# Kernel optimization log

Hardware: AMD Instinct MI355X
Metric: run time of the kernel (lower is better)

The kernel has to match this reference:

```python
import jax, jax.numpy as jnp
import numpy as np

N, E, D_IN, D_H, D_OUT = 8000, 256000, 128, 128, 64
TEMP = 10.0       # config temperature.value (non-learnable)
WEIGHT = 1.0      # config weight.value (non-learnable)
LN_EPS = 1e-5


def _gcn_conv(x, W, b, src, dst, n):
    # PyG GCNConv: add self loops, sym-normalized aggregation, then bias.
    h = x @ W
    loop = jnp.arange(n)
    s = jnp.concatenate([src, loop])
    d = jnp.concatenate([dst, loop])
    deg = jnp.zeros((n,), h.dtype).at[d].add(1.0)
    dinv = jax.lax.rsqrt(jnp.maximum(deg, 1e-12))
    norm = dinv[s] * dinv[d]                       # [E+N]
    out = jax.ops.segment_sum(h[s] * norm[:, None], d, num_segments=n)
    return out + b


def _entropy_gradient(x, A, temperature, normalize):
    # E_i = 0.5 * sum_j A_ij ||x_i - x_j||^2  (dense adjacency, as in repo)
    sq = jnp.sum(x * x, axis=1)                    # [N]
    Ax = A @ x                                     # [N,d]
    deg = A.sum(axis=1)                            # [N]
    En = 0.5 * (deg * sq + A @ sq - 2.0 * jnp.sum(x * Ax, axis=1))
    if normalize:
        En = En / (jnp.max(En) + 1e-12)
    logits = -En / temperature
    P = jax.nn.softmax(logits)
    logP = jax.nn.log_softmax(logits)
    S = -jnp.sum(P * logP)
    c = P * (logP + S) / temperature               # dS/dE_k
    # dS/dx_i = c_i*(deg_i x_i - (Ax)_i) + (A^T c)_i x_i - (A^T (c*x))_i
    ATc = A.T @ c
    return (c[:, None] * (deg[:, None] * x - Ax)
            + ATc[:, None] * x - A.T @ (c[:, None] * x))


def _layer_norm(x, gamma, beta):
    mu = jnp.mean(x, axis=-1, keepdims=True)
    var = jnp.mean(jnp.square(x - mu), axis=-1, keepdims=True)
    return (x - mu) * jax.lax.rsqrt(var + LN_EPS) * gamma + beta


def setup_inputs() -> dict:
    key = jax.random.key(0)
    ks = jax.random.split(key, 6)
    def w(k, i, o):
        return jax.random.normal(k, (i, o), jnp.float32) / np.sqrt(i).astype(np.float32)
    return {
        "x": jax.random.normal(ks[0], (N, D_IN), jnp.float32),
        "edge_index": jax.random.randint(ks[1], (2, E), 0, N),
        "W1": w(ks[2], D_IN, D_H), "b1": jnp.zeros((D_H,), jnp.float32),
        "W2": w(ks[3], D_H, D_H), "b2": jnp.zeros((D_H,), jnp.float32),
        "W_out": w(ks[4], D_H, D_OUT), "b_out": jnp.zeros((D_OUT,), jnp.float32),
        "ln_gamma": jnp.ones((D_H,), jnp.float32),
        "ln_beta": jnp.zeros((D_H,), jnp.float32),
    }


def reference(x, edge_index, W1, b1, W2, b2, W_out, b_out, ln_gamma, ln_beta):
    n = x.shape[0]
    src, dst = edge_index[0], edge_index[1]
    # dense adjacency (to_dense_adj sums duplicate edges)
    A = jnp.zeros((n, n), x.dtype).at[src, dst].add(1.0)
    for W, b in ((W1, b1), (W2, b2)):
        h = _gcn_conv(x, W, b, src, dst, n)
        eg = jax.lax.stop_gradient(_entropy_gradient(h, A, TEMP, True))
        h = h + WEIGHT * eg
        h = jax.nn.relu(h)
        x = _layer_norm(h, ln_gamma, ln_beta)
    embedding = _gcn_conv(x, W_out, b_out, src, dst, n)
    return embedding
```

## Files before the change

kernel.cpp:

```cpp
#include <hip/hip_runtime.h>
#include <hip/hip_bf16.h>

#define DH 128

static constexpr float TEMP_ = 10.0f;
static constexpr float LN_EPS_ = 1e-5f;

__device__ __forceinline__ unsigned short f2bf(float f) {
  union { float f; unsigned int i; } v; v.f = f;
  unsigned int b = v.i + 0x7FFFu + ((v.i >> 16) & 1u);
  return (unsigned short)(b >> 16);
}
__device__ __forceinline__ void dec2(unsigned int u, float& lo, float& hi) {
  union { unsigned int i; float f; } a, b;
  a.i = u << 16; b.i = u & 0xFFFF0000u;
  lo = a.f; hi = b.f;
}
__device__ __forceinline__ void dec8(uint4 u, float* o) {
  dec2(u.x, o[0], o[1]); dec2(u.y, o[2], o[3]);
  dec2(u.z, o[4], o[5]); dec2(u.w, o[6], o[7]);
}
__device__ __forceinline__ unsigned int pack2(float lo, float hi) {
  return (unsigned int)f2bf(lo) | ((unsigned int)f2bf(hi) << 16);
}

__device__ __forceinline__ float grp_sum16(float v) {
  #pragma unroll
  for (int o = 8; o > 0; o >>= 1) v += __shfl_down(v, o, 16);
  return __shfl(v, 0, 16);
}

__device__ __forceinline__ float blkred(float v, bool mx, float* s4) {
  const int t = threadIdx.x;
  #pragma unroll
  for (int o = 32; o > 0; o >>= 1) {
    float u = __shfl_down(v, o, 64);
    v = mx ? fmaxf(v, u) : v + u;
  }
  __syncthreads();
  if ((t & 63) == 0) s4[t >> 6] = v;
  __syncthreads();
  float r = mx ? fmaxf(fmaxf(s4[0], s4[1]), fmaxf(s4[2], s4[3]))
               : (s4[0] + s4[1]) + (s4[2] + s4[3]);
  __syncthreads();
  return r;
}

__global__ __launch_bounds__(256) void k_gemm1_hist(const float* __restrict__ X,
                                                    const float* __restrict__ W,
                                                    unsigned short* __restrict__ Hb,
                                                    const int* __restrict__ ei, int E,
                                                    int* cnt_d, int* cnt_s, int NT) {
  __shared__ float Ws[64 * DH];
  __shared__ float xs[16 * 128];
  const int t = threadIdx.x;
  if ((int)blockIdx.x < NT) {
    const int row0 = blockIdx.x * 16;
    const float4* xg = (const float4*)(X + row0 * 128);
    float4* xs4 = (float4*)xs;
    xs4[t] = xg[t];
    xs4[t + 256] = xg[t + 256];
    const int c = t & 127, rg = t >> 7;
    float acc[8];
    #pragma unroll
    for (int r = 0; r < 8; ++r) acc[r] = 0.f;
    for (int kt = 0; kt < 2; ++kt) {
      __syncthreads();
      for (int i = t; i < 64 * DH; i += 256) Ws[i] = W[kt * 64 * DH + i];
      __syncthreads();
      for (int k = 0; k < 64; ++k) {
        float wv = Ws[k * DH + c];
        #pragma unroll
        for (int r = 0; r < 8; ++r)
          acc[r] += xs[(rg * 8 + r) * 128 + kt * 64 + k] * wv;
      }
    }
    #pragma unroll
    for (int r = 0; r < 8; ++r)
      Hb[(row0 + rg * 8 + r) * DH + c] = f2bf(acc[r]);
  } else {
    const int nb = gridDim.x - NT;
    for (int e = (blockIdx.x - NT) * 256 + t; e < E; e += nb * 256) {
      atomicAdd(&cnt_s[ei[e]], 1);
      atomicAdd(&cnt_d[ei[E + e]], 1);
    }
  }
}

__global__ __launch_bounds__(256) void k_scan_a(const int* __restrict__ cnt_d,
                                                const int* __restrict__ cnt_s,
                                                int* off_d, int* off_s, int* bsum,
                                                float* dinv, float* dego, int n) {
  __shared__ int ws4[4];
  const int t = threadIdx.x;
  const int dir = blockIdx.x >> 5, blk = blockIdx.x & 31;
  const int* cnt = dir ? cnt_s : cnt_d;
  int* off = dir ? off_s : off_d;
  const int NPB = (n + 31) >> 5;
  const int i = blk * NPB + t;
  const bool valid = (t < NPB) && (i < n);
  int tot = valid ? cnt[i] : 0;
  const int lane = t & 63, w = t >> 6;
  int v = tot;
  #pragma unroll
  for (int o = 1; o < 64; o <<= 1) {
    int u = __shfl_up(v, o, 64);
    if (lane >= o) v += u;
  }
  if (lane == 63) ws4[w] = v;
  __syncthreads();
  int wbase = 0;
  #pragma unroll
  for (int k = 0; k < 4; ++k) wbase += (k < w) ? ws4[k] : 0;
  const int excl = wbase + v - tot;
  if (valid) {
    off[i] = excl;
    if (dir == 0) dinv[i] = rsqrtf((float)tot + 1.0f);
    else          dego[i] = (float)tot;
  }
  if (t == 0) {
    int bt = 0;
    #pragma unroll
    for (int k = 0; k < 4; ++k) bt += ws4[k];
    bsum[dir * 32 + blk] = bt;
  }
}

__global__ __launch_bounds__(256) void k_scan_b(int* cnt_d, int* cnt_s,
                                                int* off_d, int* off_s,
                                                const int* __restrict__ bsum, int n) {
  __shared__ int sb;
  const int t = threadIdx.x;
  const int dir = blockIdx.x >> 5, blk = blockIdx.x & 31;
  int* cnt = dir ? cnt_s : cnt_d;
  int* off = dir ? off_s : off_d;
  if (t == 0) {
    int s = 0;
    for (int k = 0; k < blk; ++k) s += bsum[dir * 32 + k];
    sb = s;
  }
  __syncthreads();
  const int bbase = sb;
  const int NPB = (n + 31) >> 5;
  const int i = blk * NPB + t;
  if (t < NPB && i < n) {
    off[i] = bbase + off[i];
    cnt[i] = 0;
  }
  if (t == 1 && blk == 31) {
    int s = 0;
    for (int k = 0; k < 32; ++k) s += bsum[dir * 32 + k];
    off[n] = s;
  }
}

__global__ void k_fill(const int* __restrict__ ei, int E,
                       const int* __restrict__ off_d, const int* __restrict__ off_s,
                       int* cnt_d, int* cnt_s, int* idx_d, int* idx_s) {
  int e = blockIdx.x * blockDim.x + threadIdx.x;
  if (e < E) {
    int s = ei[e], d = ei[E + e];
    int p = atomicAdd(&cnt_d[d], 1);
    idx_d[off_d[d] + p] = s;
    int q = atomicAdd(&cnt_s[s], 1);
    idx_s[off_s[s] + q] = d;
  }
}

__global__ __launch_bounds__(256) void k_conv_agg(const unsigned short* __restrict__ Hb,
                                                  const float* __restrict__ dinv,
                                                  const float* __restrict__ b,
                                                  const int* __restrict__ off_d,
                                                  const int* __restrict__ idx_d,
                                                  float* __restrict__ G,
                                                  unsigned short* __restrict__ Gb,
                                                  float* __restrict__ sq) {
  const int lane = threadIdx.x & 15;
  const int i = blockIdx.x * 16 + (threadIdx.x >> 4);
  const uint4* Hv = (const uint4*)Hb;
  const float di = dinv[i];
  float acc[8];
  {
    float t8[8]; dec8(Hv[i * 16 + lane], t8);
    #pragma unroll
    for (int k = 0; k < 8; ++k) acc[k] = di * t8[k];
  }
  int o = off_d[i];
  const int oe = off_d[i + 1];
  for (; o + 8 <= oe; o += 8) {
    int s[8]; float dv[8]; uint4 r[8];
    #pragma unroll
    for (int j = 0; j < 8; ++j) s[j] = idx_d[o + j];
    #pragma unroll
    for (int j = 0; j < 8; ++j) { r[j] = Hv[s[j] * 16 + lane]; dv[j] = dinv[s[j]]; }
    #pragma unroll
    for (int j = 0; j < 8; ++j) {
      float t8[8]; dec8(r[j], t8);
      #pragma unroll
      for (int k = 0; k < 8; ++k) acc[k] = fmaf(dv[j], t8[k], acc[k]);
    }
  }
  for (; o < oe; ++o) {
    int s = idx_d[o];
    float dvs = dinv[s];
    float t8[8]; dec8(Hv[s * 16 + lane], t8);
    #pragma unroll
    for (int k = 0; k < 8; ++k) acc[k] = fmaf(dvs, t8[k], acc[k]);
  }
  const float4 b0 = ((const float4*)b)[lane * 2];
  const float4 b1 = ((const float4*)b)[lane * 2 + 1];
  float gi[8];
  gi[0] = fmaf(di, acc[0], b0.x); gi[1] = fmaf(di, acc[1], b0.y);
  gi[2] = fmaf(di, acc[2], b0.z); gi[3] = fmaf(di, acc[3], b0.w);
  gi[4] = fmaf(di, acc[4], b1.x); gi[5] = fmaf(di, acc[5], b1.y);
  gi[6] = fmaf(di, acc[6], b1.z); gi[7] = fmaf(di, acc[7], b1.w);
  ((float4*)G)[i * 32 + lane * 2]     = make_float4(gi[0], gi[1], gi[2], gi[3]);
  ((float4*)G)[i * 32 + lane * 2 + 1] = make_float4(gi[4], gi[5], gi[6], gi[7]);
  uint4 gp;
  gp.x = pack2(gi[0], gi[1]); gp.y = pack2(gi[2], gi[3]);
  gp.z = pack2(gi[4], gi[5]); gp.w = pack2(gi[6], gi[7]);
  ((uint4*)Gb)[i * 16 + lane] = gp;
  float s2 = 0.f;
  #pragma unroll
  for (int k = 0; k < 8; ++k) s2 += gi[k] * gi[k];
  s2 = grp_sum16(s2);
  if (lane == 0) sq[i] = s2;
}

__global__ __launch_bounds__(256) void k_ax_en(const float* __restrict__ G,
                                               const unsigned short* __restrict__ Gb,
                                               const float* __restrict__ sq,
                                               const float* __restrict__ dego,
                                               const int* __restrict__ off_s,
                                               const int* __restrict__ idx_s,
                                               float* __restrict__ Ax,
                                               float* __restrict__ En) {
  const int lane = threadIdx.x & 15;
  const int i = blockIdx.x * 16 + (threadIdx.x >> 4);
  const uint4* Gv = (const uint4*)Gb;
  float axf[8];
  #pragma unroll
  for (int k = 0; k < 8; ++k) axf[k] = 0.f;
  float asq = 0.f;
  int o = off_s[i];
  const int oe = off_s[i + 1];
  for (; o + 8 <= oe; o += 8) {
    int s[8]; float qv[8]; uint4 r[8];
    #pragma unroll
    for (int j = 0; j < 8; ++j) s[j] = idx_s[o + j];
    #pragma unroll
    for (int j = 0; j < 8; ++j) { r[j] = Gv[s[j] * 16 + lane]; qv[j] = sq[s[j]]; }
    #pragma unroll
    for (int j = 0; j < 8; ++j) {
      float t8[8]; dec8(r[j], t8);
      asq += qv[j];
      #pragma unroll
      for (int k = 0; k < 8; ++k) axf[k] += t8[k];
    }
  }
  for (; o < oe; ++o) {
    int s = idx_s[o];
    float t8[8]; dec8(Gv[s * 16 + lane], t8);
    asq += sq[s];
    #pragma unroll
    for (int k = 0; k < 8; ++k) axf[k] += t8[k];
  }
  ((float4*)Ax)[i * 32 + lane * 2]     = make_float4(axf[0], axf[1], axf[2], axf[3]);
  ((float4*)Ax)[i * 32 + lane * 2 + 1] = make_float4(axf[4], axf[5], axf[6], axf[7]);
  const float4 g0 = ((const float4*)G)[i * 32 + lane * 2];
  const float4 g1 = ((const float4*)G)[i * 32 + lane * 2 + 1];
  float dot = g0.x * axf[0] + g0.y * axf[1] + g0.z * axf[2] + g0.w * axf[3]
            + g1.x * axf[4] + g1.y * axf[5] + g1.z * axf[6] + g1.w * axf[7];
  dot = grp_sum16(dot);
  if (lane == 0) En[i] = 0.5f * (dego[i] * sq[i] + asq - 2.f * dot);
}

template <int DOUT>
__global__ __launch_bounds__(256) void k_combine_gemm(const float* __restrict__ G,
                                                      const unsigned short* __restrict__ Gb,
                                                      const float* __restrict__ Ax,
                                                      const float* __restrict__ En,
                                                      const float* __restrict__ dego,
                                                      const int* __restrict__ off_d,
                                                      const int* __restrict__ idx_d,
                                                      const float* __restrict__ gamma,
                                                      const float* __restrict__ beta,
                                                      const float* __restrict__ W,
                                                      unsigned short* __restrict__ Hb,
                                                      int n) {
  __shared__ float Ws[64 * DOUT];
  __shared__ float xs[16 * 128];
  __shared__ float s4[4];
  const int t = threadIdx.x;
  float mloc = -3.0e38f;
  for (int k = t; k < n; k += 256) mloc = fmaxf(mloc, En[k]);
  const float m = blkred(mloc, true, s4);
  const float invden = -1.0f / ((m + 1e-12f) * TEMP_);
  float se = 0.f, sl = 0.f;
  for (int k = t; k < n; k += 256) {
    float li = En[k] * invden;
    float e = __expf(li);
    se += e; sl += e * li;
  }
  se = blkred(se, false, s4);
  sl = blkred(sl, false, s4);
  const float logZ = __logf(se);
  const float S = logZ - sl / se;
  const float cmul = (1.0f / se) * (1.0f / TEMP_);
  const float cadd = S - logZ;

  const int lane = t & 15;
  const int i = blockIdx.x * 16 + (t >> 4);
  const uint4* Gv = (const uint4*)Gb;
  const float4 g0 = ((const float4*)G)[i * 32 + lane * 2];
  const float4 g1 = ((const float4*)G)[i * 32 + lane * 2 + 1];
  const float gi[8] = { g0.x, g0.y, g0.z, g0.w, g1.x, g1.y, g1.z, g1.w };
  float tf[8];
  #pragma unroll
  for (int k = 0; k < 8; ++k) tf[k] = 0.f;
  float atc = 0.f;
  int o = off_d[i];
  const int oe = off_d[i + 1];
  for (; o + 8 <= oe; o += 8) {
    int s[8]; float ev[8]; uint4 r[8];
    #pragma unroll
    for (int j = 0; j < 8; ++j) s[j] = idx_d[o + j];
    #pragma unroll
    for (int j = 0; j < 8; ++j) { r[j] = Gv[s[j] * 16 + lane]; ev[j] = En[s[j]]; }
    #pragma unroll
    for (int j = 0; j < 8; ++j) {
      float ls = ev[j] * invden;
      float cs = __expf(ls) * cmul * (ls + cadd);
      atc += cs;
      float t8[8]; dec8(r[j], t8);
      #pragma unroll
      for (int k = 0; k < 8; ++k) tf[k] = fmaf(cs, t8[k], tf[k]);
    }
  }
  for (; o < oe; ++o) {
    int s = idx_d[o];
    float ls = En[s] * invden;
    float cs = __expf(ls) * cmul * (ls + cadd);
    atc += cs;
    float t8[8]; dec8(Gv[s * 16 + lane], t8);
    #pragma unroll
    for (int k = 0; k < 8; ++k) tf[k] = fmaf(cs, t8[k], tf[k]);
  }
  const float li_i = En[i] * invden;
  const float ci = __expf(li_i) * cmul * (li_i + cadd);
  const float dg = dego[i];
  const float4 a0 = ((const float4*)Ax)[i * 32 + lane * 2];
  const float4 a1 = ((const float4*)Ax)[i * 32 + lane * 2 + 1];
  const float axi[8] = { a0.x, a0.y, a0.z, a0.w, a1.x, a1.y, a1.z, a1.w };
  float v[8];
  float ssum = 0.f;
  #pragma unroll
  for (int k = 0; k < 8; ++k) {
    v[k] = fmaxf(gi[k] + ci * (dg * gi[k] - axi[k]) + atc * gi[k] - tf[k], 0.f);
    ssum += v[k];
  }
  float mu = grp_sum16(ssum) * (1.f / 128.f);
  float vsum = 0.f;
  #pragma unroll
  for (int k = 0; k < 8; ++k) {
    v[k] -= mu;
    vsum += v[k] * v[k];
  }
  float var = grp_sum16(vsum) * (1.f / 128.f);
  float rs = rsqrtf(var + LN_EPS_);
  const float4 ga0 = ((const float4*)gamma)[lane * 2];
  const float4 ga1 = ((const float4*)gamma)[lane * 2 + 1];
  const float4 be0 = ((const float4*)beta)[lane * 2];
  const float4 be1 = ((const float4*)beta)[lane * 2 + 1];
  float4 o0, o1;
  o0.x = fmaf(v[0] * rs, ga0.x, be0.x); o0.y = fmaf(v[1] * rs, ga0.y, be0.y);
  o0.z = fmaf(v[2] * rs, ga0.z, be0.z); o0.w = fmaf(v[3] * rs, ga0.w, be0.w);
  o1.x = fmaf(v[4] * rs, ga1.x, be1.x); o1.y = fmaf(v[5] * rs, ga1.y, be1.y);
  o1.z = fmaf(v[6] * rs, ga1.z, be1.z); o1.w = fmaf(v[7] * rs, ga1.w, be1.w);

  float* xrow = xs + (t >> 4) * 128 + lane * 8;
  ((float4*)xrow)[0] = o0;
  ((float4*)xrow)[1] = o1;

  const int row0 = blockIdx.x * 16;
  constexpr int RPT = (16 * DOUT) / 256;
  const int c = t % DOUT;
  const int rg = t / DOUT;
  float acc[RPT];
  #pragma unroll
  for (int r = 0; r < RPT; ++r) acc[r] = 0.f;
  for (int kt = 0; kt < 2; ++kt) {
    if (kt) __syncthreads();
    for (int idx = t; idx < 64 * DOUT; idx += 256) Ws[idx] = W[kt * 64 * DOUT + idx];
    __syncthreads();
    for (int k = 0; k < 64; ++k) {
      float wv = Ws[k * DOUT + c];
      #pragma unroll
      for (int r = 0; r < RPT; ++r)
        acc[r] += xs[(rg * RPT + r) * 128 + kt * 64 + k] * wv;
    }
  }
  #pragma unroll
  for (int r = 0; r < RPT; ++r)
    Hb[(row0 + rg * RPT + r) * DOUT + c] = f2bf(acc[r]);
}

__global__ __launch_bounds__(256) void k_final_agg(const unsigned short* __restrict__ Hb,
                                                   const float* __restrict__ dinv,
                                                   const float* __restrict__ bout,
                                                   const int* __restrict__ off_d,
                                                   const int* __restrict__ idx_d,
                                                   float* __restrict__ out) {
  const int lane = threadIdx.x & 7;
  const int i = blockIdx.x * 32 + (threadIdx.x >> 3);
  const uint4* Hv = (const uint4*)Hb;
  const float di = dinv[i];
  float acc[8];
  {
    float t8[8]; dec8(Hv[i * 8 + lane], t8);
    #pragma unroll
    for (int k = 0; k < 8; ++k) acc[k] = di * t8[k];
  }
  int o = off_d[i];
  const int oe = off_d[i + 1];
  for (; o + 8 <= oe; o += 8) {
    int s[8]; float dv[8]; uint4 r[8];
    #pragma unroll
    for (int j = 0; j < 8; ++j) s[j] = idx_d[o + j];
    #pragma unroll
    for (int j = 0; j < 8; ++j) { r[j] = Hv[s[j] * 8 + lane]; dv[j] = dinv[s[j]]; }
    #pragma unroll
    for (int j = 0; j < 8; ++j) {
      float t8[8]; dec8(r[j], t8);
      #pragma unroll
      for (int k = 0; k < 8; ++k) acc[k] = fmaf(dv[j], t8[k], acc[k]);
    }
  }
  for (; o < oe; ++o) {
    int s = idx_d[o];
    float dvs = dinv[s];
    float t8[8]; dec8(Hv[s * 8 + lane], t8);
    #pragma unroll
    for (int k = 0; k < 8; ++k) acc[k] = fmaf(dvs, t8[k], acc[k]);
  }
  const float4 b0 = ((const float4*)bout)[lane * 2];
  const float4 b1 = ((const float4*)bout)[lane * 2 + 1];
  float4 r0, r1;
  r0.x = fmaf(di, acc[0], b0.x); r0.y = fmaf(di, acc[1], b0.y);
  r0.z = fmaf(di, acc[2], b0.z); r0.w = fmaf(di, acc[3], b0.w);
  r1.x = fmaf(di, acc[4], b1.x); r1.y = fmaf(di, acc[5], b1.y);
  r1.z = fmaf(di, acc[6], b1.z); r1.w = fmaf(di, acc[7], b1.w);
  ((float4*)out)[i * 16 + lane * 2]     = r0;
  ((float4*)out)[i * 16 + lane * 2 + 1] = r1;
}

extern "C" void kernel_launch(void* const* d_in, const int* in_sizes, int n_in,
                              void* d_out, int out_size, void* d_ws, size_t ws_size,
                              hipStream_t stream) {
  const float* x    = (const float*)d_in[0];
  const int*   ei   = (const int*)d_in[1];
  const float* W1   = (const float*)d_in[2];
  const float* b1   = (const float*)d_in[3];
  const float* W2   = (const float*)d_in[4];
  const float* b2   = (const float*)d_in[5];
  const float* Wout = (const float*)d_in[6];
  const float* bout = (const float*)d_in[7];
  const float* gam  = (const float*)d_in[8];
  const float* bet  = (const float*)d_in[9];
  float* out = (float*)d_out;

  const int N = in_sizes[0] / DH;
  const int E = in_sizes[1] / 2;

  float* ws = (float*)d_ws;
  float* G  = ws;   ws += N * DH;
  float* Ax = ws;   ws += N * DH;
  float* sq = ws;   ws += N;
  float* En = ws;   ws += N;
  float* dinv = ws; ws += N;
  float* dego = ws; ws += N;
  unsigned short* Hb = (unsigned short*)ws; ws += N * DH / 2;
  unsigned short* Gb = (unsigned short*)ws; ws += N * DH / 2;
  int* cnt_d  = (int*)ws; ws += N;
  int* cnt_s  = (int*)ws; ws += N;
  int* off_d  = (int*)ws; ws += N + 4;
  int* off_s  = (int*)ws; ws += N + 4;
  int* bsum   = (int*)ws; ws += 64;
  int* idx_d  = (int*)ws; ws += E;
  int* idx_s  = (int*)ws; ws += E;

  const int NT = N / 16;

  hipMemsetAsync(cnt_d, 0, 2 * N * sizeof(int), stream);
  k_gemm1_hist<<<NT + 256, 256, 0, stream>>>(x, W1, Hb, ei, E, cnt_d, cnt_s, NT);
  k_scan_a<<<64, 256, 0, stream>>>(cnt_d, cnt_s, off_d, off_s, bsum, dinv, dego, N);
  k_scan_b<<<64, 256, 0, stream>>>(cnt_d, cnt_s, off_d, off_s, bsum, N);
  k_fill<<<(E + 255) / 256, 256, 0, stream>>>(ei, E, off_d, off_s, cnt_d, cnt_s,
                                              idx_d, idx_s);

  k_conv_agg<<<N / 16, 256, 0, stream>>>(Hb, dinv, b1, off_d, idx_d, G, Gb, sq);
  k_ax_en<<<N / 16, 256, 0, stream>>>(G, Gb, sq, dego, off_s, idx_s, Ax, En);
  k_combine_gemm<128><<<N / 16, 256, 0, stream>>>(G, Gb, Ax, En, dego, off_d,
                                                  idx_d, gam, bet, W2, Hb, N);
  k_conv_agg<<<N / 16, 256, 0, stream>>>(Hb, dinv, b2, off_d, idx_d, G, Gb, sq);
  k_ax_en<<<N / 16, 256, 0, stream>>>(G, Gb, sq, dego, off_s, idx_s, Ax, En);
  k_combine_gemm<64><<<N / 16, 256, 0, stream>>>(G, Gb, Ax, En, dego, off_d,
                                                 idx_d, gam, bet, Wout, Hb, N);
  k_final_agg<<<N / 32, 256, 0, stream>>>(Hb, dinv, bout, off_d, idx_d, out);
}
```

Before: 237.9 us.

## Precompute per-node softmax coefficients into shared memory as bf16 in combine kernel

Each block now computes the entropy-gradient coefficient c for all nodes once, stores it as bf16 in a 16 KB shared array, and reads it during the neighbor gather. This replaces a per-edge global En load plus exp. The max/sum reductions over En are vectorized with float4, and the W tile is halved to 32 rows to make room in LDS. Each block recomputes all n coefficients, which adds redundant exp work per block. The bf16 rounding of c also introduces some precision loss. The float4 loop assumes n is divisible by 4, and the shared array assumes n ≤ 8192.

```diff
diff --git a/kernel.cpp b/kernel.cpp
--- a/kernel.cpp
+++ b/kernel.cpp
@@ -10,6 +10,9 @@
   union { float f; unsigned int i; } v; v.f = f;
   unsigned int b = v.i + 0x7FFFu + ((v.i >> 16) & 1u);
   return (unsigned short)(b >> 16);
+}
+__device__ __forceinline__ float bf2f(unsigned short u) {
+  union { unsigned int i; float f; } v; v.i = ((unsigned int)u) << 16; return v.f;
 }
 __device__ __forceinline__ void dec2(unsigned int u, float& lo, float& hi) {
   union { unsigned int i; float f; } a, b;
@@ -288,19 +291,28 @@
                                                       const float* __restrict__ W,
                                                       unsigned short* __restrict__ Hb,
                                                       int n) {
-  __shared__ float Ws[64 * DOUT];
+  __shared__ unsigned short cvb[8192];
+  __shared__ float Ws[32 * DOUT];
   __shared__ float xs[16 * 128];
   __shared__ float s4[4];
   const int t = threadIdx.x;
+
+  const float4* En4 = (const float4*)En;
+  const int n4 = n >> 2;
   float mloc = -3.0e38f;
-  for (int k = t; k < n; k += 256) mloc = fmaxf(mloc, En[k]);
+  for (int k = t; k < n4; k += 256) {
+    float4 e = En4[k];
+    mloc = fmaxf(mloc, fmaxf(fmaxf(e.x, e.y), fmaxf(e.z, e.w)));
+  }
   const float m = blkred(mloc, true, s4);
   const float invden = -1.0f / ((m + 1e-12f) * TEMP_);
   float se = 0.f, sl = 0.f;
-  for (int k = t; k < n; k += 256) {
-    float li = En[k] * invden;
-    float e = __expf(li);
-    se += e; sl += e * li;
+  for (int k = t; k < n4; k += 256) {
+    float4 e = En4[k];
+    float l0 = e.x * invden, l1 = e.y * invden, l2 = e.z * invden, l3 = e.w * invden;
+    float e0 = __expf(l0), e1 = __expf(l1), e2 = __expf(l2), e3 = __expf(l3);
+    se += (e0 + e1) + (e2 + e3);
+    sl += (e0 * l0 + e1 * l1) + (e2 * l2 + e3 * l3);
   }
   se = blkred(se, false, s4);
   sl = blkred(sl, false, s4);
@@ -308,6 +320,11 @@
   const float S = logZ - sl / se;
   const float cmul = (1.0f / se) * (1.0f / TEMP_);
   const float cadd = S - logZ;
+  for (int k = t; k < n; k += 256) {
+    float ls = En[k] * invden;
+    cvb[k] = f2bf(__expf(ls) * cmul * (ls + cadd));
+  }
+  __syncthreads();
 
   const int lane = t & 15;
   const int i = blockIdx.x * 16 + (t >> 4);
@@ -322,32 +339,28 @@
   int o = off_d[i];
   const int oe = off_d[i + 1];
   for (; o + 8 <= oe; o += 8) {
-    int s[8]; float ev[8]; uint4 r[8];
+    int s[8]; float cs[8]; uint4 r[8];
     #pragma unroll
     for (int j = 0; j < 8; ++j) s[j] = idx_d[o + j];
     #pragma unroll
-    for (int j = 0; j < 8; ++j) { r[j] = Gv[s[j] * 16 + lane]; ev[j] = En[s[j]]; }
+    for (int j = 0; j < 8; ++j) { r[j] = Gv[s[j] * 16 + lane]; cs[j] = bf2f(cvb[s[j]]); }
     #pragma unroll
     for (int j = 0; j < 8; ++j) {
-      float ls = ev[j] * invden;
-      float cs = __expf(ls) * cmul * (ls + cadd);
-      atc += cs;
+      atc += cs[j];
       float t8[8]; dec8(r[j], t8);
       #pragma unroll
-      for (int k = 0; k < 8; ++k) tf[k] = fmaf(cs, t8[k], tf[k]);
+      for (int k = 0; k < 8; ++k) tf[k] = fmaf(cs[j], t8[k], tf[k]);
     }
   }
   for (; o < oe; ++o) {
     int s = idx_d[o];
-    float ls = En[s] * invden;
-    float cs = __expf(ls) * cmul * (ls + cadd);
+    float cs = bf2f(cvb[s]);
     atc += cs;
     float t8[8]; dec8(Gv[s * 16 + lane], t8);
     #pragma unroll
     for (int k = 0; k < 8; ++k) tf[k] = fmaf(cs, t8[k], tf[k]);
   }
-  const float li_i = En[i] * invden;
-  const float ci = __expf(li_i) * cmul * (li_i + cadd);
+  const float ci = bf2f(cvb[i]);
   const float dg = dego[i];
   const float4 a0 = ((const float4*)Ax)[i * 32 + lane * 2];
   const float4 a1 = ((const float4*)Ax)[i * 32 + lane * 2 + 1];
@@ -389,15 +402,15 @@
   float acc[RPT];
   #pragma unroll
   for (int r = 0; r < RPT; ++r) acc[r] = 0.f;
-  for (int kt = 0; kt < 2; ++kt) {
+  for (int kt = 0; kt < 4; ++kt) {
     if (kt) __syncthreads();
-    for (int idx = t; idx < 64 * DOUT; idx += 256) Ws[idx] = W[kt * 64 * DOUT + idx];
+    for (int idx = t; idx < 32 * DOUT; idx += 256) Ws[idx] = W[kt * 32 * DOUT + idx];
     __syncthreads();
-    for (int k = 0; k < 64; ++k) {
+    for (int k = 0; k < 32; ++k) {
       float wv = Ws[k * DOUT + c];
       #pragma unroll
       for (int r = 0; r < RPT; ++r)
-        acc[r] += xs[(rg * RPT + r) * 128 + kt * 64 + k] * wv;
+        acc[r] += xs[(rg * RPT + r) * 128 + kt * 32 + k] * wv;
     }
   }
   #pragma unroll
```

Result: slower. 254.8 us (+7.1%).

## Prescale GEMM outputs by dinv and move GEMM1 into edge-fill kernel

Applied to the files above, without the earlier changes.

Each GEMM now stores dinv[row]*h in bf16, so the three aggregation kernels no longer gather dinv[src] per neighbour and just sum the rows. Because GEMM1 now needs dinv, it moves out of the histogram kernel and runs alongside the CSR fill kernel, and the histogram gets its own launch. This removes one random gather per edge in each aggregation, at the cost of restructuring how the preprocessing kernels overlap. Rounding to bf16 after the scaling slightly changes numerics.

```diff
diff --git a/kernel.cpp b/kernel.cpp
--- a/kernel.cpp
+++ b/kernel.cpp
@@ -46,44 +46,10 @@
   return r;
 }
 
-__global__ __launch_bounds__(256) void k_gemm1_hist(const float* __restrict__ X,
-                                                    const float* __restrict__ W,
-                                                    unsigned short* __restrict__ Hb,
-                                                    const int* __restrict__ ei, int E,
-                                                    int* cnt_d, int* cnt_s, int NT) {
-  __shared__ float Ws[64 * DH];
-  __shared__ float xs[16 * 128];
-  const int t = threadIdx.x;
-  if ((int)blockIdx.x < NT) {
-    const int row0 = blockIdx.x * 16;
-    const float4* xg = (const float4*)(X + row0 * 128);
-    float4* xs4 = (float4*)xs;
-    xs4[t] = xg[t];
-    xs4[t + 256] = xg[t + 256];
-    const int c = t & 127, rg = t >> 7;
-    float acc[8];
-    #pragma unroll
-    for (int r = 0; r < 8; ++r) acc[r] = 0.f;
-    for (int kt = 0; kt < 2; ++kt) {
-      __syncthreads();
-      for (int i = t; i < 64 * DH; i += 256) Ws[i] = W[kt * 64 * DH + i];
-      __syncthreads();
-      for (int k = 0; k < 64; ++k) {
-        float wv = Ws[k * DH + c];
-        #pragma unroll
-        for (int r = 0; r < 8; ++r)
-          acc[r] += xs[(rg * 8 + r) * 128 + kt * 64 + k] * wv;
-      }
-    }
-    #pragma unroll
-    for (int r = 0; r < 8; ++r)
-      Hb[(row0 + rg * 8 + r) * DH + c] = f2bf(acc[r]);
-  } else {
-    const int nb = gridDim.x - NT;
-    for (int e = (blockIdx.x - NT) * 256 + t; e < E; e += nb * 256) {
-      atomicAdd(&cnt_s[ei[e]], 1);
-      atomicAdd(&cnt_d[ei[E + e]], 1);
-    }
+__global__ void k_hist(const int* __restrict__ ei, int E, int* cnt_d, int* cnt_s) {
+  for (int e = blockIdx.x * 256 + threadIdx.x; e < E; e += gridDim.x * 256) {
+    atomicAdd(&cnt_s[ei[e]], 1);
+    atomicAdd(&cnt_d[ei[E + e]], 1);
   }
 }
 
@@ -154,16 +120,53 @@
   }
 }
 
-__global__ void k_fill(const int* __restrict__ ei, int E,
-                       const int* __restrict__ off_d, const int* __restrict__ off_s,
-                       int* cnt_d, int* cnt_s, int* idx_d, int* idx_s) {
-  int e = blockIdx.x * blockDim.x + threadIdx.x;
-  if (e < E) {
-    int s = ei[e], d = ei[E + e];
-    int p = atomicAdd(&cnt_d[d], 1);
-    idx_d[off_d[d] + p] = s;
-    int q = atomicAdd(&cnt_s[s], 1);
-    idx_s[off_s[s] + q] = d;
+__global__ __launch_bounds__(256) void k_gemm1_fill(const float* __restrict__ X,
+                                                    const float* __restrict__ W,
+                                                    const float* __restrict__ dinv,
+                                                    unsigned short* __restrict__ Hb,
+                                                    const int* __restrict__ ei, int E,
+                                                    const int* __restrict__ off_d,
+                                                    const int* __restrict__ off_s,
+                                                    int* cnt_d, int* cnt_s,
+                                                    int* idx_d, int* idx_s, int NT) {
+  __shared__ float Ws[64 * DH];
+  __shared__ float xs[16 * 128];
+  const int t = threadIdx.x;
+  if ((int)blockIdx.x < NT) {
+    const int row0 = blockIdx.x * 16;
+    const float4* xg = (const float4*)(X + row0 * 128);
+    float4* xs4 = (float4*)xs;
+    xs4[t] = xg[t];
+    xs4[t + 256] = xg[t + 256];
+    const int c = t & 127, rg = t >> 7;
+    float acc[8];
+    #pragma unroll
+    for (int r = 0; r < 8; ++r) acc[r] = 0.f;
+    for (int kt = 0; kt < 2; ++kt) {
+      __syncthreads();
+      for (int i = t; i < 64 * DH; i += 256) Ws[i] = W[kt * 64 * DH + i];
+      __syncthreads();
+      for (int k = 0; k < 64; ++k) {
+        float wv = Ws[k * DH + c];
+        #pragma unroll
+        for (int r = 0; r < 8; ++r)
+          acc[r] += xs[(rg * 8 + r) * 128 + kt * 64 + k] * wv;
+      }
+    }
+    #pragma unroll
+    for (int r = 0; r < 8; ++r) {
+      const int row = row0 + rg * 8 + r;
+      Hb[row * DH + c] = f2bf(dinv[row] * acc[r]);
+    }
+  } else {
+    const int nb = gridDim.x - NT;
+    for (int e = (blockIdx.x - NT) * 256 + t; e < E; e += nb * 256) {
+      int s = ei[e], d = ei[E + e];
+      int p = atomicAdd(&cnt_d[d], 1);
+      idx_d[off_d[d] + p] = s;
+      int q = atomicAdd(&cnt_s[s], 1);
+      idx_s[off_s[s] + q] = d;
+    }
   }
 }
 
@@ -180,32 +183,27 @@
   const uint4* Hv = (const uint4*)Hb;
   const float di = dinv[i];
   float acc[8];
-  {
-    float t8[8]; dec8(Hv[i * 16 + lane], t8);
-    #pragma unroll
-    for (int k = 0; k < 8; ++k) acc[k] = di * t8[k];
-  }
+  dec8(Hv[i * 16 + lane], acc);
   int o = off_d[i];
   const int oe = off_d[i + 1];
   for (; o + 8 <= oe; o += 8) {
-    int s[8]; float dv[8]; uint4 r[8];
+    int s[8]; uint4 r[8];
     #pragma unroll
     for (int j = 0; j < 8; ++j) s[j] = idx_d[o + j];
     #pragma unroll
-    for (int j = 0; j < 8; ++j) { r[j] = Hv[s[j] * 16 + lane]; dv[j] = dinv[s[j]]; }
+    for (int j = 0; j < 8; ++j) r[j] = Hv[s[j] * 16 + lane];
     #pragma unroll
     for (int j = 0; j < 8; ++j) {
       float t8[8]; dec8(r[j], t8);
       #pragma unroll
-      for (int k = 0; k < 8; ++k) acc[k] = fmaf(dv[j], t8[k], acc[k]);
+      for (int k = 0; k < 8; ++k) acc[k] += t8[k];
     }
   }
   for (; o < oe; ++o) {
     int s = idx_d[o];
-    float dvs = dinv[s];
     float t8[8]; dec8(Hv[s * 16 + lane], t8);
     #pragma unroll
-    for (int k = 0; k < 8; ++k) acc[k] = fmaf(dvs, t8[k], acc[k]);
+    for (int k = 0; k < 8; ++k) acc[k] += t8[k];
   }
   const float4 b0 = ((const float4*)b)[lane * 2];
   const float4 b1 = ((const float4*)b)[lane * 2 + 1];
@@ -281,6 +279,7 @@
                                                       const float* __restrict__ Ax,
                                                       const float* __restrict__ En,
                                                       const float* __restrict__ dego,
+                                                      const float* __restrict__ dinv,
                                                       const int* __restrict__ off_d,
                                                       const int* __restrict__ idx_d,
                                                       const float* __restrict__ gamma,
@@ -401,8 +400,10 @@
     }
   }
   #pragma unroll
-  for (int r = 0; r < RPT; ++r)
-    Hb[(row0 + rg * RPT + r) * DOUT + c] = f2bf(acc[r]);
+  for (int r = 0; r < RPT; ++r) {
+    const int row = row0 + rg * RPT + r;
+    Hb[row * DOUT + c] = f2bf(dinv[row] * acc[r]);
+  }
 }
 
 __global__ __launch_bounds__(256) void k_final_agg(const unsigned short* __restrict__ Hb,
@@ -416,32 +417,27 @@
   const uint4* Hv = (const uint4*)Hb;
   const float di = dinv[i];
   float acc[8];
-  {
-    float t8[8]; dec8(Hv[i * 8 + lane], t8);
-    #pragma unroll
-    for (int k = 0; k < 8; ++k) acc[k] = di * t8[k];
-  }
+  dec8(Hv[i * 8 + lane], acc);
   int o = off_d[i];
   const int oe = off_d[i + 1];
   for (; o + 8 <= oe; o += 8) {
-    int s[8]; float dv[8]; uint4 r[8];
+    int s[8]; uint4 r[8];
     #pragma unroll
     for (int j = 0; j < 8; ++j) s[j] = idx_d[o + j];
     #pragma unroll
-    for (int j = 0; j < 8; ++j) { r[j] = Hv[s[j] * 8 + lane]; dv[j] = dinv[s[j]]; }
+    for (int j = 0; j < 8; ++j) r[j] = Hv[s[j] * 8 + lane];
     #pragma unroll
     for (int j = 0; j < 8; ++j) {
       float t8[8]; dec8(r[j], t8);
       #pragma unroll
-      for (int k = 0; k < 8; ++k) acc[k] = fmaf(dv[j], t8[k], acc[k]);
+      for (int k = 0; k < 8; ++k) acc[k] += t8[k];
     }
   }
   for (; o < oe; ++o) {
     int s = idx_d[o];
-    float dvs = dinv[s];
     float t8[8]; dec8(Hv[s * 8 + lane], t8);
     #pragma unroll
-    for (int k = 0; k < 8; ++k) acc[k] = fmaf(dvs, t8[k], acc[k]);
+    for (int k = 0; k < 8; ++k) acc[k] += t8[k];
   }
   const float4 b0 = ((const float4*)bout)[lane * 2];
   const float4 b1 = ((const float4*)bout)[lane * 2 + 1];
@@ -492,19 +488,20 @@
   const int NT = N / 16;
 
   hipMemsetAsync(cnt_d, 0, 2 * N * sizeof(int), stream);
-  k_gemm1_hist<<<NT + 256, 256, 0, stream>>>(x, W1, Hb, ei, E, cnt_d, cnt_s, NT);
+  k_hist<<<256, 256, 0, stream>>>(ei, E, cnt_d, cnt_s);
   k_scan_a<<<64, 256, 0, stream>>>(cnt_d, cnt_s, off_d, off_s, bsum, dinv, dego, N);
   k_scan_b<<<64, 256, 0, stream>>>(cnt_d, cnt_s, off_d, off_s, bsum, N);
-  k_fill<<<(E + 255) / 256, 256, 0, stream>>>(ei, E, off_d, off_s, cnt_d, cnt_s,
-                                              idx_d, idx_s);
+  k_gemm1_fill<<<NT + (E + 255) / 256, 256, 0, stream>>>(x, W1, dinv, Hb, ei, E,
+                                                         off_d, off_s, cnt_d, cnt_s,
+                                                         idx_d, idx_s, NT);
 
   k_conv_agg<<<N / 16, 256, 0, stream>>>(Hb, dinv, b1, off_d, idx_d, G, Gb, sq);
   k_ax_en<<<N / 16, 256, 0, stream>>>(G, Gb, sq, dego, off_s, idx_s, Ax, En);
-  k_combine_gemm<128><<<N / 16, 256, 0, stream>>>(G, Gb, Ax, En, dego, off_d,
+  k_combine_gemm<128><<<N / 16, 256, 0, stream>>>(G, Gb, Ax, En, dego, dinv, off_d,
                                                   idx_d, gam, bet, W2, Hb, N);
   k_conv_agg<<<N / 16, 256, 0, stream>>>(Hb, dinv, b2, off_d, idx_d, G, Gb, sq);
   k_ax_en<<<N / 16, 256, 0, stream>>>(G, Gb, sq, dego, off_s, idx_s, Ax, En);
-  k_combine_gemm<64><<<N / 16, 256, 0, stream>>>(G, Gb, Ax, En, dego, off_d,
+  k_combine_gemm<64><<<N / 16, 256, 0, stream>>>(G, Gb, Ax, En, dego, dinv, off_d,
                                                  idx_d, gam, bet, Wout, Hb, N);
   k_final_agg<<<N / 32, 256, 0, stream>>>(Hb, dinv, bout, off_d, idx_d, out);
 }
```

Measured after the change: 236.8 us. No clear change (-0.5%).
